# Kernel optimization log

Measured on AMD Instinct MI355X. Metric: run time of the kernel, lower is better.

The kernel has to match this reference:

```python
import jax, jax.numpy as jnp
import numpy as np

N = 6144      # total atoms
F = 128       # hidden_dim
NB = 48       # number of molecules (batch segments)
LONG_RANGE_SCALE = 1.0


def setup_inputs() -> dict:
    key = jax.random.key(0)
    ks = jax.random.split(key, 16)
    s = 1.0 / np.sqrt(F)
    return {
        "h0": jax.random.normal(ks[0], (N, F), jnp.float32),
        "h1": jax.random.normal(ks[1], (N, 3, F), jnp.float32),
        "pos": jax.random.normal(ks[2], (N, 3), jnp.float32),
        "batch": jnp.sort(jax.random.randint(ks[3], (N,), 0, NB)),
        "qW1": jax.random.normal(ks[4], (F, F // 2), jnp.float32) * s,
        "qb1": jnp.zeros((F // 2,), jnp.float32),
        "qW2": jax.random.normal(ks[5], (F // 2, 1), jnp.float32) * s,
        "qb2": jnp.zeros((1,), jnp.float32),
        "cW1": jax.random.normal(ks[6], (F, F // 2), jnp.float32) * s,
        "cb1": jnp.zeros((F // 2,), jnp.float32),
        "cW2": jax.random.normal(ks[7], (F // 2, 1), jnp.float32) * s,
        "cb2": jnp.zeros((1,), jnp.float32),
        "muW": jax.random.normal(ks[8], (F, 1), jnp.float32) * s,
    }


def reference(h0, h1, pos, batch, qW1, qb1, qW2, qb2, cW1, cb1, cW2, cb2, muW):
    n = pos.shape[0]
    # pairwise geometry
    batch_mask = batch[:, None] == batch[None, :]                 # (N,N) bool
    diff = pos[:, None, :] - pos[None, :, :]                      # (N,N,3)
    dist_sq = jnp.sum(diff * diff, axis=-1)                       # (N,N)
    dist = jnp.sqrt(dist_sq + 1e-8)
    valid = batch_mask & ~jnp.eye(n, dtype=bool)
    validf = valid.astype(dist.dtype)

    energy = jnp.zeros((), dist.dtype)

    # --- Coulomb (use_charge) ---
    q = jax.nn.silu(h0 @ qW1 + qb1) @ qW2 + qb2                   # (N,1)
    q_sum = jax.ops.segment_sum(q, batch, num_segments=NB)        # (NB,1)
    cnt = jax.ops.segment_sum(jnp.ones((n, 1), q.dtype), batch, num_segments=NB)
    q_mean = q_sum / jnp.maximum(cnt, 1.0)                        # scatter_mean
    q = q - q_mean[batch]                                         # per-molecule neutrality
    qq = q @ q.T                                                  # (N,N)
    f_taper = 1.0 - jnp.exp(-0.5 * dist)
    E_coul = jnp.sum(qq / dist * f_taper * validf)
    energy = energy + 0.5 * E_coul * 14.399

    # --- van der Waals (use_vdw) ---
    c6 = jax.nn.softplus(jax.nn.silu(h0 @ cW1 + cb1) @ cW2 + cb2)  # (N,1), >0
    c6_ij = jnp.sqrt(c6 @ c6.T)                                    # (N,N)
    r6 = dist_sq ** 3
    E_vdw = -jnp.sum(c6_ij / (r6 + 20.0) * validf)
    energy = energy + 0.5 * E_vdw

    # --- dipole-dipole (use_dipole) ---
    mu = (h1 @ muW)[..., 0]                                        # (N,3)
    mu_dot_mu = mu @ mu.T                                          # (N,N)
    n_ij = diff / (dist[..., None] + 1e-8)                         # (N,N,3)
    mu_dot_n_i = jnp.einsum("id,ijd->ij", mu, n_ij)
    mu_dot_n_j = jnp.einsum("jd,ijd->ij", mu, n_ij)
    inv_r3 = 1.0 / (dist_sq * dist + 10.0)
    E_dip = jnp.sum((mu_dot_mu - 3.0 * mu_dot_n_i * mu_dot_n_j) * inv_r3 * validf)
    energy = energy + 0.5 * E_dip

    return energy * LONG_RANGE_SCALE
```

## Files before the change

### kernel.cpp

```cpp
#include <hip/hip_runtime.h>
#include <math.h>

#define F 128
#define H 64
#define HH 32
#define AT 64
#define NBMOL 48
#define CAP 256
#define SPLIT 16

__device__ __forceinline__ float silu_f(float x) {
    return x / (1.0f + __expf(-x));
}
__device__ __forceinline__ float softplus_f(float x) {
    return fmaxf(x, 0.0f) + log1pf(__expf(-fabsf(x)));
}
__device__ __forceinline__ float frcp(float x) {
    return __builtin_amdgcn_rcpf(x);
}
__device__ __forceinline__ float dot4(float4 a, float4 b) {
    return fmaf(a.x, b.x, fmaf(a.y, b.y, fmaf(a.z, b.z, a.w * b.w)));
}

__global__ __launch_bounds__(256, 3) void k_mlp(
    const float* __restrict__ h0,
    const float* __restrict__ qW1, const float* __restrict__ qb1,
    const float* __restrict__ qW2,
    const float* __restrict__ cW1, const float* __restrict__ cb1,
    const float* __restrict__ cW2,
    float* __restrict__ part,
    float* __restrict__ out, int N)
{
    __shared__ float4 sW4[HH * 32];
    __shared__ float4 sX4[AT * 32];
    __shared__ float red[4][AT];

    const int b = blockIdx.x;
    const int tid = threadIdx.x;
    if (b == 0 && tid == 0) out[0] = 0.0f;

    const int tile  = b >> 2;
    const int net   = b & 1;
    const int hhalf = (b >> 1) & 1;
    const float* __restrict__ W1 = net ? cW1 : qW1;
    const float* __restrict__ b1 = net ? cb1 : qb1;
    const float* __restrict__ W2 = net ? cW2 : qW2;

    for (int idx = tid; idx < HH * F; idx += 256) {
        int f = idx >> 5;
        int hh = idx & 31;
        float val = W1[f * H + hhalf * HH + hh];
        int f4 = f >> 2, fi = f & 3;
        ((float*)&sW4[hh * 32 + (f4 ^ ((hh >> 1) & 7))])[fi] = val;
    }
    const float4* __restrict__ h0v = (const float4*)h0;
    for (int idx = tid; idx < AT * 32; idx += 256) {
        int a = idx >> 5, f4 = idx & 31;
        int row = min(tile * AT + a, N - 1);
        sX4[a * 32 + (f4 ^ ((a >> 2) & 7))] = h0v[(size_t)row * 32 + f4];
    }
    __syncthreads();

    const int ag = tid & 15;
    const int hg = tid >> 4;
    const int swx = ag & 7;
    const int sww = hg & 7;
    const int h0i = hhalf * HH + 2 * hg;

    float z[4][2];
    {
        float b0 = b1[h0i], b1v = b1[h0i + 1];
        #pragma unroll
        for (int j = 0; j < 4; ++j) { z[j][0] = b0; z[j][1] = b1v; }
    }

    #pragma unroll 4
    for (int f4 = 0; f4 < 32; ++f4) {
        float4 w0 = sW4[(2 * hg) * 32 + (f4 ^ sww)];
        float4 w1 = sW4[(2 * hg + 1) * 32 + (f4 ^ sww)];
        #pragma unroll
        for (int j = 0; j < 4; ++j) {
            float4 x = sX4[(4 * ag + j) * 32 + (f4 ^ swx)];
            z[j][0] += dot4(x, w0);
            z[j][1] += dot4(x, w1);
        }
    }

    const float w2a = W2[h0i], w2b = W2[h0i + 1];
    float p[4];
    #pragma unroll
    for (int j = 0; j < 4; ++j)
        p[j] = fmaf(silu_f(z[j][0]), w2a, silu_f(z[j][1]) * w2b);

    #pragma unroll
    for (int j = 0; j < 4; ++j) {
        p[j] += __shfl_xor(p[j], 16);
        p[j] += __shfl_xor(p[j], 32);
    }
    const int wv = tid >> 6, lane = tid & 63;
    if (lane < 16) {
        #pragma unroll
        for (int j = 0; j < 4; ++j) red[wv][4 * lane + j] = p[j];
    }
    __syncthreads();
    if (tid < AT) {
        float s = red[0][tid] + red[1][tid] + red[2][tid] + red[3][tid];
        int atom = tile * AT + tid;
        if (atom < N) part[(size_t)(net * 2 + hhalf) * N + atom] = s;
    }
}

__global__ __launch_bounds__(256, 8) void k_dip(
    const float* __restrict__ h1, const float* __restrict__ muW,
    float* __restrict__ mu, int nrows)
{
    const int slot = threadIdx.x >> 4;
    const int l = threadIdx.x & 15;
    int row = blockIdx.x * 16 + slot;
    if (row < nrows) {
        const float4* rp = (const float4*)(h1 + (size_t)row * F);
        const float4* mp = (const float4*)muW;
        float pm = dot4(rp[2 * l], mp[2 * l]) +
                   dot4(rp[2 * l + 1], mp[2 * l + 1]);
        #pragma unroll
        for (int off = 1; off < 16; off <<= 1) pm += __shfl_xor(pm, off);
        if (l == 0) mu[row] = pm;
    }
}

__global__ __launch_bounds__(256) void k_pair(
    const float* __restrict__ pos,
    const int* __restrict__ batch,
    const float* __restrict__ part,
    const float* __restrict__ mu,
    const float* __restrict__ qb2, const float* __restrict__ cb2,
    float* __restrict__ out, int N)
{
    const int b = blockIdx.x;
    const int s = blockIdx.y;
    const int tid = threadIdx.x;

    __shared__ int sst, sen;
    __shared__ float sq[CAP], sc[CAP], sp[3 * CAP], sm[3 * CAP];
    __shared__ float red[4];

    if (tid == 0) { sst = 0; sen = 0; }
    __syncthreads();
    for (int k = tid; k < N; k += 256) {
        int bk = batch[k];
        if (bk == b) {
            if (k == 0 || batch[k - 1] != b) sst = k;
            if (k == N - 1 || batch[k + 1] != b) sen = k + 1;
        }
    }
    __syncthreads();
    const int st = sst;
    const int n = sen - sst;

    const float* __restrict__ p0 = part;
    const float* __restrict__ p1 = part + N;
    const float* __restrict__ p2 = part + 2 * (size_t)N;
    const float* __restrict__ p3 = part + 3 * (size_t)N;
    const float qb2v = qb2[0], cb2v = cb2[0];

    float e_c = 0.f, e_v = 0.f, e_d = 0.f;

    if (n > 1 && n <= CAP) {
        float partsum = 0.f;
        for (int k = tid; k < n; k += 256) {
            float qv = p0[st + k] + p1[st + k] + qb2v;
            sq[k] = qv; partsum += qv;
            sc[k] = sqrtf(softplus_f(p2[st + k] + p3[st + k] + cb2v));
        }
        for (int k = tid; k < 3 * n; k += 256) {
            sp[k] = pos[3 * st + k];
            sm[k] = mu[3 * st + k];
        }
        #pragma unroll
        for (int off = 32; off > 0; off >>= 1)
            partsum += __shfl_xor(partsum, off);
        if ((tid & 63) == 0) red[tid >> 6] = partsum;
        __syncthreads();
        const float mean = (red[0] + red[1] + red[2] + red[3]) / (float)n;

        const int r = tid >> 4;
        const int c = tid & 15;
        for (int il = s + SPLIT * r; il < n; il += SPLIT * 16) {
            const float qi = sq[il] - mean;
            const float sci = sc[il];
            const float xi = sp[3 * il], yi = sp[3 * il + 1], zi = sp[3 * il + 2];
            const float mxi = sm[3 * il], myi = sm[3 * il + 1], mzi = sm[3 * il + 2];
            for (int jl = c; jl < n; jl += 16) {
                if (jl == il) continue;
                float dx = xi - sp[3 * jl], dy = yi - sp[3 * jl + 1],
                      dz = zi - sp[3 * jl + 2];
                float ds0 = fmaf(dx, dx, fmaf(dy, dy, dz * dz));
                float d = sqrtf(ds0 + 1e-8f);
                float inv_d = frcp(d);
                float qj = sq[jl] - mean;
                e_c = fmaf(qi * qj * inv_d, 1.0f - __expf(-0.5f * d), e_c);
                float r6 = ds0 * ds0 * ds0;
                e_v = fmaf(sci * sc[jl], frcp(r6 + 20.0f), e_v);
                float smx = sm[3 * jl], smy = sm[3 * jl + 1], smz = sm[3 * jl + 2];
                float mdm = fmaf(mxi, smx, fmaf(myi, smy, mzi * smz));
                float mdni = fmaf(mxi, dx, fmaf(myi, dy, mzi * dz)) * inv_d;
                float mdnj = fmaf(smx, dx, fmaf(smy, dy, smz * dz)) * inv_d;
                e_d = fmaf(mdm - 3.0f * mdni * mdnj,
                           frcp(fmaf(ds0, d, 10.0f)), e_d);
            }
        }
    } else if (n > CAP) {
        float partsum = 0.f;
        for (int k = tid; k < n; k += 256)
            partsum += p0[st + k] + p1[st + k] + qb2v;
        #pragma unroll
        for (int off = 32; off > 0; off >>= 1)
            partsum += __shfl_xor(partsum, off);
        if ((tid & 63) == 0) red[tid >> 6] = partsum;
        __syncthreads();
        const float mean = (red[0] + red[1] + red[2] + red[3]) / (float)n;
        const int r = tid >> 4, c = tid & 15;
        for (int j0 = 0; j0 < n; j0 += CAP) {
            const int chunk = min(CAP, n - j0);
            __syncthreads();
            for (int k = tid; k < chunk; k += 256) {
                int j = st + j0 + k;
                sq[k] = p0[j] + p1[j] + qb2v;
                sc[k] = sqrtf(softplus_f(p2[j] + p3[j] + cb2v));
            }
            for (int k = tid; k < 3 * chunk; k += 256) {
                sp[k] = pos[3 * (st + j0) + k];
                sm[k] = mu[3 * (st + j0) + k];
            }
            __syncthreads();
            for (int il = s + SPLIT * r; il < n; il += SPLIT * 16) {
                const int i = st + il;
                const float qi = p0[i] + p1[i] + qb2v - mean;
                const float sci = sqrtf(softplus_f(p2[i] + p3[i] + cb2v));
                const float xi = pos[i * 3], yi = pos[i * 3 + 1], zi = pos[i * 3 + 2];
                const float mxi = mu[i * 3], myi = mu[i * 3 + 1], mzi = mu[i * 3 + 2];
                for (int jl = c; jl < chunk; jl += 16) {
                    if (j0 + jl == il) continue;
                    float dx = xi - sp[3 * jl], dy = yi - sp[3 * jl + 1],
                          dz = zi - sp[3 * jl + 2];
                    float ds0 = fmaf(dx, dx, fmaf(dy, dy, dz * dz));
                    float d = sqrtf(ds0 + 1e-8f);
                    float inv_d = frcp(d);
                    float qj = sq[jl] - mean;
                    e_c = fmaf(qi * qj * inv_d, 1.0f - __expf(-0.5f * d), e_c);
                    float r6 = ds0 * ds0 * ds0;
                    e_v = fmaf(sci * sc[jl], frcp(r6 + 20.0f), e_v);
                    float smx = sm[3 * jl], smy = sm[3 * jl + 1], smz = sm[3 * jl + 2];
                    float mdm = fmaf(mxi, smx, fmaf(myi, smy, mzi * smz));
                    float mdni = fmaf(mxi, dx, fmaf(myi, dy, mzi * dz)) * inv_d;
                    float mdnj = fmaf(smx, dx, fmaf(smy, dy, smz * dz)) * inv_d;
                    e_d = fmaf(mdm - 3.0f * mdni * mdnj,
                               frcp(fmaf(ds0, d, 10.0f)), e_d);
                }
            }
        }
    }

    float vv = fmaf(7.1995f, e_c, fmaf(-0.5f, e_v, 0.5f * e_d));
    #pragma unroll
    for (int off = 32; off > 0; off >>= 1) vv += __shfl_xor(vv, off);
    __syncthreads();
    if ((tid & 63) == 0) red[tid >> 6] = vv;
    __syncthreads();
    if (tid == 0) atomicAdd(out, red[0] + red[1] + red[2] + red[3]);
}

extern "C" void kernel_launch(void* const* d_in, const int* in_sizes, int n_in,
                              void* d_out, int out_size, void* d_ws, size_t ws_size,
                              hipStream_t stream) {
    const float* h0  = (const float*)d_in[0];
    const float* h1  = (const float*)d_in[1];
    const float* pos = (const float*)d_in[2];
    const int*   batch = (const int*)d_in[3];
    const float* qW1 = (const float*)d_in[4];
    const float* qb1 = (const float*)d_in[5];
    const float* qW2 = (const float*)d_in[6];
    const float* qb2 = (const float*)d_in[7];
    const float* cW1 = (const float*)d_in[8];
    const float* cb1 = (const float*)d_in[9];
    const float* cW2 = (const float*)d_in[10];
    const float* cb2 = (const float*)d_in[11];
    const float* muW = (const float*)d_in[12];
    float* out = (float*)d_out;
    const int N = in_sizes[0] / F;

    float* ws = (float*)d_ws;
    float* part = ws;
    float* mu   = part + 4 * (size_t)N;

    const int ntile = (N + AT - 1) / AT;
    const int nrows = 3 * N;

    k_mlp<<<4 * ntile, 256, 0, stream>>>(h0, qW1, qb1, qW2, cW1, cb1, cW2,
                                         part, out, N);
    k_dip<<<(nrows + 15) / 16, 256, 0, stream>>>(h1, muW, mu, nrows);
    k_pair<<<dim3(NBMOL, SPLIT), 256, 0, stream>>>(pos, batch, part, mu,
                                                   qb2, cb2, out, N);
}
```

Baseline: 116.6 us.

## Fuse dipole projection into MLP kernel and compute full hidden width per block

Merges the mu projection kernel into the MLP kernel and has each block compute all 64 hidden units rather than splitting into halves. The bias, softplus and sqrt are applied in the MLP epilogue. The pair kernel now reads ready-made q and sqrt(c6) and runs with half as many split blocks. This removes one launch and redundant h0 tile loads, but raises register and LDS pressure and reduces pair-kernel parallelism.

Result: no change. 114.9 us (-1.5%).

```diff
diff --git a/kernel.cpp b/kernel.cpp
--- a/kernel.cpp
+++ b/kernel.cpp
@@ -3,11 +3,10 @@
 
 #define F 128
 #define H 64
-#define HH 32
 #define AT 64
 #define NBMOL 48
 #define CAP 256
-#define SPLIT 16
+#define SPLIT 8
 
 __device__ __forceinline__ float silu_f(float x) {
     return x / (1.0f + __expf(-x));
@@ -22,16 +21,18 @@
     return fmaf(a.x, b.x, fmaf(a.y, b.y, fmaf(a.z, b.z, a.w * b.w)));
 }
 
-__global__ __launch_bounds__(256, 3) void k_mlp(
-    const float* __restrict__ h0,
+__global__ __launch_bounds__(256, 2) void k_mlp(
+    const float* __restrict__ h0, const float* __restrict__ h1,
     const float* __restrict__ qW1, const float* __restrict__ qb1,
-    const float* __restrict__ qW2,
+    const float* __restrict__ qW2, const float* __restrict__ qb2,
     const float* __restrict__ cW1, const float* __restrict__ cb1,
-    const float* __restrict__ cW2,
-    float* __restrict__ part,
-    float* __restrict__ out, int N)
+    const float* __restrict__ cW2, const float* __restrict__ cb2,
+    const float* __restrict__ muW,
+    float* __restrict__ q_raw, float* __restrict__ sqc6,
+    float* __restrict__ mu,
+    float* __restrict__ out, int N, int nrows)
 {
-    __shared__ float4 sW4[HH * 32];
+    __shared__ float4 sW4[H * 32];
     __shared__ float4 sX4[AT * 32];
     __shared__ float red[4][AT];
 
@@ -39,19 +40,18 @@
     const int tid = threadIdx.x;
     if (b == 0 && tid == 0) out[0] = 0.0f;
 
-    const int tile  = b >> 2;
-    const int net   = b & 1;
-    const int hhalf = (b >> 1) & 1;
+    const int net  = b & 1;
+    const int tile = b >> 1;
     const float* __restrict__ W1 = net ? cW1 : qW1;
     const float* __restrict__ b1 = net ? cb1 : qb1;
     const float* __restrict__ W2 = net ? cW2 : qW2;
 
-    for (int idx = tid; idx < HH * F; idx += 256) {
-        int f = idx >> 5;
-        int hh = idx & 31;
-        float val = W1[f * H + hhalf * HH + hh];
+    for (int idx = tid; idx < H * F; idx += 256) {
+        int f = idx >> 6;
+        int h = idx & 63;
+        float val = W1[f * H + h];
         int f4 = f >> 2, fi = f & 3;
-        ((float*)&sW4[hh * 32 + (f4 ^ ((hh >> 1) & 7))])[fi] = val;
+        ((float*)&sW4[h * 32 + (f4 ^ ((h >> 1) & 7))])[fi] = val;
     }
     const float4* __restrict__ h0v = (const float4*)h0;
     for (int idx = tid; idx < AT * 32; idx += 256) {
@@ -63,35 +63,40 @@
 
     const int ag = tid & 15;
     const int hg = tid >> 4;
-    const int swx = ag & 7;
-    const int sww = hg & 7;
-    const int h0i = hhalf * HH + 2 * hg;
-
-    float z[4][2];
-    {
-        float b0 = b1[h0i], b1v = b1[h0i + 1];
-        #pragma unroll
-        for (int j = 0; j < 4; ++j) { z[j][0] = b0; z[j][1] = b1v; }
+
+    float z[4][4];
+    #pragma unroll
+    for (int k = 0; k < 4; ++k) {
+        float bv = b1[4 * hg + k];
+        #pragma unroll
+        for (int j = 0; j < 4; ++j) z[j][k] = bv;
     }
 
     #pragma unroll 4
     for (int f4 = 0; f4 < 32; ++f4) {
-        float4 w0 = sW4[(2 * hg) * 32 + (f4 ^ sww)];
-        float4 w1 = sW4[(2 * hg + 1) * 32 + (f4 ^ sww)];
+        float4 w[4];
+        #pragma unroll
+        for (int k = 0; k < 4; ++k) {
+            int hr = 4 * hg + k;
+            w[k] = sW4[hr * 32 + (f4 ^ ((hr >> 1) & 7))];
+        }
         #pragma unroll
         for (int j = 0; j < 4; ++j) {
-            float4 x = sX4[(4 * ag + j) * 32 + (f4 ^ swx)];
-            z[j][0] += dot4(x, w0);
-            z[j][1] += dot4(x, w1);
-        }
-    }
-
-    const float w2a = W2[h0i], w2b = W2[h0i + 1];
+            int ar = 4 * ag + j;
+            float4 x = sX4[ar * 32 + (f4 ^ ((ar >> 2) & 7))];
+            #pragma unroll
+            for (int k = 0; k < 4; ++k) z[j][k] += dot4(x, w[k]);
+        }
+    }
+
     float p[4];
     #pragma unroll
-    for (int j = 0; j < 4; ++j)
-        p[j] = fmaf(silu_f(z[j][0]), w2a, silu_f(z[j][1]) * w2b);
-
+    for (int j = 0; j < 4; ++j) {
+        p[j] = 0.f;
+        #pragma unroll
+        for (int k = 0; k < 4; ++k)
+            p[j] = fmaf(silu_f(z[j][k]), W2[4 * hg + k], p[j]);
+    }
     #pragma unroll
     for (int j = 0; j < 4; ++j) {
         p[j] += __shfl_xor(p[j], 16);
@@ -106,34 +111,34 @@
     if (tid < AT) {
         float s = red[0][tid] + red[1][tid] + red[2][tid] + red[3][tid];
         int atom = tile * AT + tid;
-        if (atom < N) part[(size_t)(net * 2 + hhalf) * N + atom] = s;
-    }
-}
-
-__global__ __launch_bounds__(256, 8) void k_dip(
-    const float* __restrict__ h1, const float* __restrict__ muW,
-    float* __restrict__ mu, int nrows)
-{
-    const int slot = threadIdx.x >> 4;
-    const int l = threadIdx.x & 15;
-    int row = blockIdx.x * 16 + slot;
-    if (row < nrows) {
-        const float4* rp = (const float4*)(h1 + (size_t)row * F);
-        const float4* mp = (const float4*)muW;
-        float pm = dot4(rp[2 * l], mp[2 * l]) +
-                   dot4(rp[2 * l + 1], mp[2 * l + 1]);
-        #pragma unroll
-        for (int off = 1; off < 16; off <<= 1) pm += __shfl_xor(pm, off);
-        if (l == 0) mu[row] = pm;
+        if (atom < N) {
+            if (net == 0) q_raw[atom] = s + qb2[0];
+            else          sqc6[atom]  = sqrtf(softplus_f(s + cb2[0]));
+        }
+    }
+
+    const int slot = tid >> 4;
+    const int l = tid & 15;
+    const float4* mp = (const float4*)muW;
+    const float4 m0 = mp[2 * l], m1 = mp[2 * l + 1];
+    #pragma unroll
+    for (int ppp = 0; ppp < 6; ++ppp) {
+        int row = b * 96 + ppp * 16 + slot;
+        if (row < nrows) {
+            const float4* rp = (const float4*)(h1 + (size_t)row * F);
+            float pm = dot4(rp[2 * l], m0) + dot4(rp[2 * l + 1], m1);
+            #pragma unroll
+            for (int off = 1; off < 16; off <<= 1) pm += __shfl_xor(pm, off);
+            if (l == 0) mu[row] = pm;
+        }
     }
 }
 
 __global__ __launch_bounds__(256) void k_pair(
     const float* __restrict__ pos,
     const int* __restrict__ batch,
-    const float* __restrict__ part,
+    const float* __restrict__ q_raw, const float* __restrict__ sqc6,
     const float* __restrict__ mu,
-    const float* __restrict__ qb2, const float* __restrict__ cb2,
     float* __restrict__ out, int N)
 {
     const int b = blockIdx.x;
@@ -157,20 +162,14 @@
     const int st = sst;
     const int n = sen - sst;
 
-    const float* __restrict__ p0 = part;
-    const float* __restrict__ p1 = part + N;
-    const float* __restrict__ p2 = part + 2 * (size_t)N;
-    const float* __restrict__ p3 = part + 3 * (size_t)N;
-    const float qb2v = qb2[0], cb2v = cb2[0];
-
     float e_c = 0.f, e_v = 0.f, e_d = 0.f;
 
     if (n > 1 && n <= CAP) {
         float partsum = 0.f;
         for (int k = tid; k < n; k += 256) {
-            float qv = p0[st + k] + p1[st + k] + qb2v;
+            float qv = q_raw[st + k];
             sq[k] = qv; partsum += qv;
-            sc[k] = sqrtf(softplus_f(p2[st + k] + p3[st + k] + cb2v));
+            sc[k] = sqc6[st + k];
         }
         for (int k = tid; k < 3 * n; k += 256) {
             sp[k] = pos[3 * st + k];
@@ -211,8 +210,7 @@
         }
     } else if (n > CAP) {
         float partsum = 0.f;
-        for (int k = tid; k < n; k += 256)
-            partsum += p0[st + k] + p1[st + k] + qb2v;
+        for (int k = tid; k < n; k += 256) partsum += q_raw[st + k];
         #pragma unroll
         for (int off = 32; off > 0; off >>= 1)
             partsum += __shfl_xor(partsum, off);
@@ -224,9 +222,8 @@
             const int chunk = min(CAP, n - j0);
             __syncthreads();
             for (int k = tid; k < chunk; k += 256) {
-                int j = st + j0 + k;
-                sq[k] = p0[j] + p1[j] + qb2v;
-                sc[k] = sqrtf(softplus_f(p2[j] + p3[j] + cb2v));
+                sq[k] = q_raw[st + j0 + k];
+                sc[k] = sqc6[st + j0 + k];
             }
             for (int k = tid; k < 3 * chunk; k += 256) {
                 sp[k] = pos[3 * (st + j0) + k];
@@ -235,8 +232,8 @@
             __syncthreads();
             for (int il = s + SPLIT * r; il < n; il += SPLIT * 16) {
                 const int i = st + il;
-                const float qi = p0[i] + p1[i] + qb2v - mean;
-                const float sci = sqrtf(softplus_f(p2[i] + p3[i] + cb2v));
+                const float qi = q_raw[i] - mean;
+                const float sci = sqc6[i];
                 const float xi = pos[i * 3], yi = pos[i * 3 + 1], zi = pos[i * 3 + 2];
                 const float mxi = mu[i * 3], myi = mu[i * 3 + 1], mzi = mu[i * 3 + 2];
                 for (int jl = c; jl < chunk; jl += 16) {
@@ -290,15 +287,16 @@
     const int N = in_sizes[0] / F;
 
     float* ws = (float*)d_ws;
-    float* part = ws;
-    float* mu   = part + 4 * (size_t)N;
+    float* q_raw = ws;
+    float* sqc6  = q_raw + N;
+    float* mu    = sqc6 + N;
 
     const int ntile = (N + AT - 1) / AT;
     const int nrows = 3 * N;
 
-    k_mlp<<<4 * ntile, 256, 0, stream>>>(h0, qW1, qb1, qW2, cW1, cb1, cW2,
-                                         part, out, N);
-    k_dip<<<(nrows + 15) / 16, 256, 0, stream>>>(h1, muW, mu, nrows);
-    k_pair<<<dim3(NBMOL, SPLIT), 256, 0, stream>>>(pos, batch, part, mu,
-                                                   qb2, cb2, out, N);
-}
+    k_mlp<<<2 * ntile, 256, 0, stream>>>(h0, h1, qW1, qb1, qW2, qb2,
+                                         cW1, cb1, cW2, cb2, muW,
+                                         q_raw, sqc6, mu, out, N, nrows);
+    k_pair<<<dim3(NBMOL, SPLIT), 256, 0, stream>>>(pos, batch, q_raw, sqc6,
+                                                   mu, out, N);
+}
```
